# Optimization experiments

Hardware: AMD Instinct MI355X
Metric: run time of the kernel (lower is better)

Reference implementation:

```python
import jax, jax.numpy as jnp
import numpy as np

def setup_inputs() -> dict:
    key = jax.random.key(0)
    k0, k1, k2, k3 = jax.random.split(key, 4)
    B, L, D, E, Dg = 2, 2048, 2048, 8, 256  # Dg = D // E
    x = jax.random.normal(k0, (B, L, D), dtype=jnp.float32)
    Wg = jax.random.normal(k1, (E, D), dtype=jnp.float32) * 0.02     # gate: Linear(D, E)
    Wd = jax.random.normal(k2, (E, Dg, D), dtype=jnp.float32) * 0.02  # down: Linear(D, Dg) per expert
    Wu = jax.random.normal(k3, (E, D, Dg), dtype=jnp.float32) * 0.02  # up:   Linear(Dg, D) per expert
    return {"x": x, "Wg": Wg, "Wd": Wd, "Wu": Wu, "k": 2}

def reference(x, Wg, Wd, Wu, k):
    B, L, D = x.shape
    E = Wg.shape[0]
    T = B * L
    xf = x.reshape(T, D)
    # gate scores: sigmoid(x @ Wg^T), then top-k gate values G and expert indices I
    S = jax.nn.sigmoid(xf @ Wg.T)            # [T, E]
    G, I = jax.lax.top_k(S, k)               # [T, k], [T, k]
    # combine weights per token per expert (zero for unselected experts);
    # equivalent to the original's one_hot + per-expert gather/scatter-add.
    w = jnp.zeros((T, E), x.dtype).at[jnp.arange(T)[:, None], I].add(G)  # [T, E]
    # down: sum_e w[t,e] * (Wd[e] @ x[t])
    down = jnp.einsum('te,egd,td->tg', w, Wd, xf)   # [T, Dg]
    # inner model is identity
    # up: sum_e w[t,e] * (Wu[e] @ down[t])
    up = jnp.einsum('te,edg,tg->td', w, Wu, down)   # [T, D]
    return up.reshape(B, L, D)
```

## Files before the change

### kernel.cpp

```cpp
#include <hip/hip_runtime.h>
#include <stdint.h>

#define T_TOK 4096
#define DIM   2048
#define NEXP  8
#define DG    256
#define TOPK  2

#define BM 64
#define BN 128
#define BKU 64
#define NROWS  (T_TOK*TOPK + NEXP*BM)
#define NBLK_M (NROWS/BM)

typedef __attribute__((ext_vector_type(8))) short short8;
typedef __attribute__((ext_vector_type(4))) float f32x4;

static __device__ __forceinline__ short f2bf(float f) {
    union { float f; uint32_t u; } v{f};
    uint32_t r = v.u + 0x7fffu + ((v.u >> 16) & 1u);
    return (short)(r >> 16);
}
static __device__ __forceinline__ float b2f(short s) {
    union { uint32_t u; float f; } v{((uint32_t)(unsigned short)s) << 16};
    return v.f;
}

#define GLD16(g, l) \
    __builtin_amdgcn_global_load_lds((const __attribute__((address_space(1))) void*)(g), \
                                     (__attribute__((address_space(3))) void*)(l), 16, 0, 0)

__global__ __launch_bounds__(256) void gateconv_kernel(const float* __restrict__ x,
                                                       const float* __restrict__ Wg,
                                                       const float* __restrict__ Wd,
                                                       const float* __restrict__ Wu,
                                                       int* __restrict__ gidx,
                                                       float* __restrict__ gval,
                                                       short* __restrict__ x_bf,
                                                       short* __restrict__ Wd_bf,
                                                       short* __restrict__ Wu_bf)
{
    if (blockIdx.x >= 1024) {
        const int n4 = NEXP * DG * DIM / 4;
        int i = (blockIdx.x - 1024) * 256 + threadIdx.x;
        const float* s; short* d; int j;
        if (i < n4) { s = Wd; d = Wd_bf; j = i; }
        else        { s = Wu; d = Wu_bf; j = i - n4; }
        float4 v = ((const float4*)s)[j];
        short4 o;
        o.x = f2bf(v.x); o.y = f2bf(v.y); o.z = f2bf(v.z); o.w = f2bf(v.w);
        ((short4*)d)[j] = o;
        return;
    }

    int token = blockIdx.x * 4 + (threadIdx.x >> 6);
    int lane  = threadIdx.x & 63;
    const float4* xr = (const float4*)(x + (size_t)token * DIM);

    float4 xv[8];
#pragma unroll
    for (int i = 0; i < 8; i++) xv[i] = xr[lane + 64 * i];

    short4* xb = (short4*)(x_bf + (size_t)token * DIM);
#pragma unroll
    for (int i = 0; i < 8; i++) {
        short4 o;
        o.x = f2bf(xv[i].x); o.y = f2bf(xv[i].y);
        o.z = f2bf(xv[i].z); o.w = f2bf(xv[i].w);
        xb[lane + 64 * i] = o;
    }

    float acc[NEXP];
#pragma unroll
    for (int e = 0; e < NEXP; e++) {
        const float4* wr = (const float4*)(Wg + e * DIM);
        float a = 0.0f;
#pragma unroll
        for (int i = 0; i < 8; i++) {
            float4 w = wr[lane + 64 * i];
            a += xv[i].x * w.x + xv[i].y * w.y + xv[i].z * w.z + xv[i].w * w.w;
        }
        acc[e] = a;
    }

#pragma unroll
    for (int m = 1; m < 64; m <<= 1) {
#pragma unroll
        for (int e = 0; e < NEXP; e++) acc[e] += __shfl_xor(acc[e], m, 64);
    }

    if (lane == 0) {
        float sg[NEXP];
#pragma unroll
        for (int e = 0; e < NEXP; e++) sg[e] = 1.0f / (1.0f + expf(-acc[e]));
        int i0 = 0;
#pragma unroll
        for (int e = 1; e < NEXP; e++) if (sg[e] > sg[i0]) i0 = e;
        int i1 = (i0 == 0) ? 1 : 0;
#pragma unroll
        for (int e = 0; e < NEXP; e++) if (e != i0 && e != i1 && sg[e] > sg[i1]) i1 = e;
        gidx[2 * token + 0] = i0;
        gidx[2 * token + 1] = i1;
        gval[2 * token + 0] = sg[i0];
        gval[2 * token + 1] = sg[i1];
    }
}

__global__ __launch_bounds__(1024) void bucket_kernel(const int* __restrict__ gidx,
                                                      int* __restrict__ rowtok,
                                                      int* __restrict__ rowpos,
                                                      int* __restrict__ seg_off)
{
    __shared__ int cnt[NEXP];
    __shared__ int cur[NEXP];
    int tid = threadIdx.x, lane = tid & 63;
    if (tid < NEXP) cnt[tid] = 0;
    __syncthreads();

    int e_[8];
#pragma unroll
    for (int r = 0; r < 8; r++) e_[r] = gidx[r * 1024 + tid];

    int mycnt = 0;
#pragma unroll
    for (int r = 0; r < 8; r++) {
        int e = e_[r];
#pragma unroll
        for (int ee = 0; ee < NEXP; ee++) {
            unsigned long long m = __ballot(e == ee);
            if (lane == ee) mycnt += (int)__popcll(m);
        }
    }
    if (lane < NEXP) atomicAdd(&cnt[lane], mycnt);
    __syncthreads();

    if (tid == 0) {
        int o = 0;
        for (int e = 0; e < NEXP; e++) {
            seg_off[e] = o;
            cur[e] = o;
            o += ((cnt[e] + BM - 1) / BM) * BM;
        }
        seg_off[NEXP] = o;
    }
    __syncthreads();

    for (int r = tid; r < NROWS; r += 1024) rowtok[r] = -1;
    __syncthreads();

#pragma unroll
    for (int r = 0; r < 8; r++) {
        int idx = r * 1024 + tid;
        int e = e_[r];
#pragma unroll
        for (int ee = 0; ee < NEXP; ee++) {
            unsigned long long m = __ballot(e == ee);
            if (m == 0) continue;
            int leader = __ffsll((unsigned long long)m) - 1;
            int base = 0;
            if (lane == leader) base = atomicAdd(&cur[ee], (int)__popcll(m));
            base = __shfl(base, leader, 64);
            if (e == ee) {
                int pos = base + (int)__popcll(m & ((1ull << lane) - 1ull));
                rowtok[pos] = idx >> 1;
                rowpos[idx] = pos;
            }
        }
    }
}

#define AS3 __attribute__((address_space(3)))

#define VMCNT(N) asm volatile("s_waitcnt vmcnt(" #N ")" ::: "memory")
#define BAR()    __builtin_amdgcn_s_barrier()

#define STAGE(B_) do { \
    GLD16(agA0, lA_##B_##_0); \
    GLD16(agA1, lA_##B_##_1); \
    GLD16(agB0, lB_##B_##_0); \
    GLD16(agB1, lB_##B_##_1); \
    GLD16(agB2, lB_##B_##_2); \
    GLD16(agB3, lB_##B_##_3); \
    agA0 += BKU; agA1 += BKU; \
    agB0 += BKU; agB1 += BKU; agB2 += BKU; agB3 += BKU; \
} while (0)

#define COMP(B_) do { \
    short8 a00 = *(const short8*)&As[B_][am0][c0]; \
    short8 a10 = *(const short8*)&As[B_][am1][c0]; \
    short8 b00 = *(const short8*)&Bs[B_][bn0][c0]; \
    short8 b10 = *(const short8*)&Bs[B_][bn1][c0]; \
    short8 b20 = *(const short8*)&Bs[B_][bn2][c0]; \
    short8 b30 = *(const short8*)&Bs[B_][bn3][c0]; \
    short8 a01 = *(const short8*)&As[B_][am0][c1]; \
    short8 a11 = *(const short8*)&As[B_][am1][c1]; \
    short8 b01 = *(const short8*)&Bs[B_][bn0][c1]; \
    short8 b11 = *(const short8*)&Bs[B_][bn1][c1]; \
    short8 b21 = *(const short8*)&Bs[B_][bn2][c1]; \
    short8 b31 = *(const short8*)&Bs[B_][bn3][c1]; \
    acc[0][0] = __builtin_amdgcn_mfma_f32_16x16x32_bf16(a00, b00, acc[0][0], 0, 0, 0); \
    acc[0][1] = __builtin_amdgcn_mfma_f32_16x16x32_bf16(a00, b10, acc[0][1], 0, 0, 0); \
    acc[0][2] = __builtin_amdgcn_mfma_f32_16x16x32_bf16(a00, b20, acc[0][2], 0, 0, 0); \
    acc[0][3] = __builtin_amdgcn_mfma_f32_16x16x32_bf16(a00, b30, acc[0][3], 0, 0, 0); \
    acc[1][0] = __builtin_amdgcn_mfma_f32_16x16x32_bf16(a10, b00, acc[1][0], 0, 0, 0); \
    acc[1][1] = __builtin_amdgcn_mfma_f32_16x16x32_bf16(a10, b10, acc[1][1], 0, 0, 0); \
    acc[1][2] = __builtin_amdgcn_mfma_f32_16x16x32_bf16(a10, b20, acc[1][2], 0, 0, 0); \
    acc[1][3] = __builtin_amdgcn_mfma_f32_16x16x32_bf16(a10, b30, acc[1][3], 0, 0, 0); \
    acc[0][0] = __builtin_amdgcn_mfma_f32_16x16x32_bf16(a01, b01, acc[0][0], 0, 0, 0); \
    acc[0][1] = __builtin_amdgcn_mfma_f32_16x16x32_bf16(a01, b11, acc[0][1], 0, 0, 0); \
    acc[0][2] = __builtin_amdgcn_mfma_f32_16x16x32_bf16(a01, b21, acc[0][2], 0, 0, 0); \
    acc[0][3] = __builtin_amdgcn_mfma_f32_16x16x32_bf16(a01, b31, acc[0][3], 0, 0, 0); \
    acc[1][0] = __builtin_amdgcn_mfma_f32_16x16x32_bf16(a11, b01, acc[1][0], 0, 0, 0); \
    acc[1][1] = __builtin_amdgcn_mfma_f32_16x16x32_bf16(a11, b11, acc[1][1], 0, 0, 0); \
    acc[1][2] = __builtin_amdgcn_mfma_f32_16x16x32_bf16(a11, b21, acc[1][2], 0, 0, 0); \
    acc[1][3] = __builtin_amdgcn_mfma_f32_16x16x32_bf16(a11, b31, acc[1][3], 0, 0, 0); \
} while (0)

__global__ __launch_bounds__(256) void gemm_down_kernel(const short* __restrict__ A,
                                                        const short* __restrict__ B,
                                                        const int* __restrict__ rowtok,
                                                        const int* __restrict__ seg_off,
                                                        short* __restrict__ C)
{
    constexpr int K = DIM, Ntot = DG;
    __shared__ __align__(16) short As[2][BM][BKU];
    __shared__ __align__(16) short Bs[2][BN][BKU];

    int d = blockIdx.x;
    int lid = (d & 7) * 34 + (d >> 3);
    int bx = lid >> 1, by = lid & 1;

    int row0 = bx * BM;
    int total = seg_off[NEXP];
    if (row0 >= total) return;
    int e = 0;
    while (row0 >= seg_off[e + 1]) ++e;
    int n0 = by * BN;

    int tid = threadIdx.x;
    int w = tid >> 6, l = tid & 63;

    int srow = (w << 3) + (l >> 3);
    int sc   = ((l & 7) ^ ((l >> 3) & 7)) << 3;

    int ta0 = rowtok[row0 + srow];      if (ta0 < 0) ta0 = 0;
    int ta1 = rowtok[row0 + 32 + srow]; if (ta1 < 0) ta1 = 0;
    const short* agA0 = A + (size_t)ta0 * K + sc;
    const short* agA1 = A + (size_t)ta1 * K + sc;
    const short* be = B + (size_t)e * Ntot * K + (size_t)n0 * K;
    const short* agB0 = be + (size_t)(srow     ) * K + sc;
    const short* agB1 = be + (size_t)(srow + 32) * K + sc;
    const short* agB2 = be + (size_t)(srow + 64) * K + sc;
    const short* agB3 = be + (size_t)(srow + 96) * K + sc;

    auto lA_0_0 = (AS3 void*)&As[0][(w << 3)     ][0];
    auto lA_0_1 = (AS3 void*)&As[0][(w << 3) + 32][0];
    auto lA_1_0 = (AS3 void*)&As[1][(w << 3)     ][0];
    auto lA_1_1 = (AS3 void*)&As[1][(w << 3) + 32][0];
    auto lB_0_0 = (AS3 void*)&Bs[0][(w << 3)     ][0];
    auto lB_0_1 = (AS3 void*)&Bs[0][(w << 3) + 32][0];
    auto lB_0_2 = (AS3 void*)&Bs[0][(w << 3) + 64][0];
    auto lB_0_3 = (AS3 void*)&Bs[0][(w << 3) + 96][0];
    auto lB_1_0 = (AS3 void*)&Bs[1][(w << 3)     ][0];
    auto lB_1_1 = (AS3 void*)&Bs[1][(w << 3) + 32][0];
    auto lB_1_2 = (AS3 void*)&Bs[1][(w << 3) + 64][0];
    auto lB_1_3 = (AS3 void*)&Bs[1][(w << 3) + 96][0];

    int mlane = l & 15, qlane = l >> 4;
    int wm = w >> 1, wn = w & 1;
    int c0 = (qlane ^ (mlane & 7)) << 3;
    int c1 = c0 ^ 32;
    int am0 = wm * 32 + mlane, am1 = am0 + 16;
    int bn0 = wn * 64 + mlane, bn1 = bn0 + 16, bn2 = bn0 + 32, bn3 = bn0 + 48;

    f32x4 acc[2][4] = {};

    constexpr int NT = K / BKU;
    STAGE(0);
    STAGE(1);
#pragma unroll 1
    for (int t = 0; t < NT - 2; t += 2) {
        VMCNT(6); BAR();
        COMP(0);
        BAR();
        STAGE(0);
        VMCNT(6); BAR();
        COMP(1);
        BAR();
        if (t + 3 < NT) STAGE(1);
    }
    VMCNT(6); BAR();
    COMP(0);
    BAR();
    VMCNT(0); BAR();
    COMP(1);

#pragma unroll
    for (int i = 0; i < 2; i++) {
        int rbase = row0 + wm * 32 + i * 16 + qlane * 4;
#pragma unroll
        for (int j = 0; j < 4; j++) {
            int col = n0 + wn * 64 + j * 16 + mlane;
#pragma unroll
            for (int r = 0; r < 4; r++)
                C[(size_t)(rbase + r) * Ntot + col] = f2bf(acc[i][j][r]);
        }
    }
}

#undef STAGE

#define STAGE_B(B_) do { \
    GLD16(agB0, lB_##B_##_0); \
    GLD16(agB1, lB_##B_##_1); \
    GLD16(agB2, lB_##B_##_2); \
    GLD16(agB3, lB_##B_##_3); \
    agB0 += BKU; agB1 += BKU; agB2 += BKU; agB3 += BKU; \
} while (0)

#define STAGE_A(B_, kb) do { \
    short8 v0 = *(const short8*)(dr00 + (kb)); \
    short8 v1 = *(const short8*)(dr01 + (kb)); \
    short8 u0 = *(const short8*)(dr10 + (kb)); \
    short8 u1 = *(const short8*)(dr11 + (kb)); \
    short8 o0, o1; \
    _Pragma("unroll") \
    for (int j = 0; j < 8; j++) { \
        o0[j] = f2bf(g00 * b2f(v0[j]) + g01 * b2f(v1[j])); \
        o1[j] = f2bf(g10 * b2f(u0[j]) + g11 * b2f(u1[j])); \
    } \
    *(short8*)&As[B_][srow     ][cl] = o0; \
    *(short8*)&As[B_][srow + 32][cl] = o1; \
} while (0)

__global__ __launch_bounds__(256) void gemm_up_kernel(const short* __restrict__ dr,
                                                      const short* __restrict__ B,
                                                      const int* __restrict__ rowtok,
                                                      const int* __restrict__ rowpos,
                                                      const float* __restrict__ gval,
                                                      const int* __restrict__ seg_off,
                                                      short* __restrict__ C)
{
    constexpr int K = DG, Ntot = DIM;
    __shared__ __align__(16) short As[2][BM][BKU];
    __shared__ __align__(16) short Bs[2][BN][BKU];

    int d = blockIdx.x;
    int lid = (d & 7) * 272 + (d >> 3);
    int bx = lid % NBLK_M;
    int by = lid / NBLK_M;

    int row0 = bx * BM;
    int total = seg_off[NEXP];
    if (row0 >= total) return;
    int e = 0;
    while (row0 >= seg_off[e + 1]) ++e;
    int n0 = by * BN;

    int tid = threadIdx.x;
    int w = tid >> 6, l = tid & 63;

    int srow = (w << 3) + (l >> 3);
    int sc   = ((l & 7) ^ ((l >> 3) & 7)) << 3;
    int cl   = (l & 7) << 3;

    int t0 = rowtok[row0 + srow];      if (t0 < 0) t0 = 0;
    int t1 = rowtok[row0 + 32 + srow]; if (t1 < 0) t1 = 0;
    int   p00 = rowpos[2 * t0], p01 = rowpos[2 * t0 + 1];
    int   p10 = rowpos[2 * t1], p11 = rowpos[2 * t1 + 1];
    float g00 = gval[2 * t0],   g01 = gval[2 * t0 + 1];
    float g10 = gval[2 * t1],   g11 = gval[2 * t1 + 1];
    const short* dr00 = dr + (size_t)p00 * DG + sc;
    const short* dr01 = dr + (size_t)p01 * DG + sc;
    const short* dr10 = dr + (size_t)p10 * DG + sc;
    const short* dr11 = dr + (size_t)p11 * DG + sc;

    const short* be = B + (size_t)e * Ntot * K + (size_t)n0 * K;
    const short* agB0 = be + (size_t)(srow     ) * K + sc;
    const short* agB1 = be + (size_t)(srow + 32) * K + sc;
    const short* agB2 = be + (size_t)(srow + 64) * K + sc;
    const short* agB3 = be + (size_t)(srow + 96) * K + sc;

    auto lB_0_0 = (AS3 void*)&Bs[0][(w << 3)     ][0];
    auto lB_0_1 = (AS3 void*)&Bs[0][(w << 3) + 32][0];
    auto lB_0_2 = (AS3 void*)&Bs[0][(w << 3) + 64][0];
    auto lB_0_3 = (AS3 void*)&Bs[0][(w << 3) + 96][0];
    auto lB_1_0 = (AS3 void*)&Bs[1][(w << 3)     ][0];
    auto lB_1_1 = (AS3 void*)&Bs[1][(w << 3) + 32][0];
    auto lB_1_2 = (AS3 void*)&Bs[1][(w << 3) + 64][0];
    auto lB_1_3 = (AS3 void*)&Bs[1][(w << 3) + 96][0];

    int mlane = l & 15, qlane = l >> 4;
    int wm = w >> 1, wn = w & 1;
    int c0 = (qlane ^ (mlane & 7)) << 3;
    int c1 = c0 ^ 32;
    int am0 = wm * 32 + mlane, am1 = am0 + 16;
    int bn0 = wn * 64 + mlane, bn1 = bn0 + 16, bn2 = bn0 + 32, bn3 = bn0 + 48;

    f32x4 acc[2][4] = {};

    STAGE_A(0, 0); STAGE_B(0);
    __syncthreads();
    STAGE_A(1, BKU); STAGE_B(1);
    COMP(0);
    __syncthreads();
    STAGE_A(0, 2 * BKU); STAGE_B(0);
    COMP(1);
    __syncthreads();
    STAGE_A(1, 3 * BKU); STAGE_B(1);
    COMP(0);
    __syncthreads();
    COMP(1);

#pragma unroll
    for (int i = 0; i < 2; i++) {
        int rbase = row0 + wm * 32 + i * 16 + qlane * 4;
#pragma unroll
        for (int j = 0; j < 4; j++) {
            int col = n0 + wn * 64 + j * 16 + mlane;
#pragma unroll
            for (int r = 0; r < 4; r++)
                C[(size_t)(rbase + r) * Ntot + col] = f2bf(acc[i][j][r]);
        }
    }
}

#undef STAGE_A
#undef STAGE_B
#undef COMP
#undef AS3

__global__ __launch_bounds__(256) void combine2_kernel(const short* __restrict__ ur,
                                                       const int* __restrict__ rowpos,
                                                       const float* __restrict__ gval,
                                                       float* __restrict__ out)
{
    int i = blockIdx.x * 256 + threadIdx.x;
    int t = i >> 9;
    int c = (i & 511) * 4;
    int   p0 = rowpos[2 * t], p1 = rowpos[2 * t + 1];
    float g0 = gval[2 * t],   g1 = gval[2 * t + 1];
    short4 u0 = *(const short4*)&ur[(size_t)p0 * DIM + c];
    short4 u1 = *(const short4*)&ur[(size_t)p1 * DIM + c];
    float4 o;
    o.x = g0 * b2f(u0.x) + g1 * b2f(u1.x);
    o.y = g0 * b2f(u0.y) + g1 * b2f(u1.y);
    o.z = g0 * b2f(u0.z) + g1 * b2f(u1.z);
    o.w = g0 * b2f(u0.w) + g1 * b2f(u1.w);
    *(float4*)&out[(size_t)t * DIM + c] = o;
}

extern "C" void kernel_launch(void* const* d_in, const int* in_sizes, int n_in,
                              void* d_out, int out_size, void* d_ws, size_t ws_size,
                              hipStream_t stream) {
    const float* x  = (const float*)d_in[0];
    const float* Wg = (const float*)d_in[1];
    const float* Wd = (const float*)d_in[2];
    const float* Wu = (const float*)d_in[3];
    float* out = (float*)d_out;

    char* p = (char*)d_ws;
    int*   gidx    = (int*)(p + 0);
    float* gval    = (float*)(p + 32768);
    int*   rowtok  = (int*)(p + 65536);
    int*   rowpos  = (int*)(p + 100352);
    int*   seg_off = (int*)(p + 133120);
    short* x_bf    = (short*)(p + 133376);
    short* Wd_bf   = (short*)(p + 133376 + 16777216);
    short* Wu_bf   = Wd_bf + 4194304;
    short* dr_bf   = Wu_bf + 4194304;
    short* ur_bf   = dr_bf + (size_t)NROWS * DG;

    gateconv_kernel<<<9216, 256, 0, stream>>>(x, Wg, Wd, Wu, gidx, gval, x_bf, Wd_bf, Wu_bf);
    bucket_kernel<<<1, 1024, 0, stream>>>(gidx, rowtok, rowpos, seg_off);
    gemm_down_kernel<<<NBLK_M * (DG / BN), 256, 0, stream>>>(x_bf, Wd_bf, rowtok, seg_off, dr_bf);
    gemm_up_kernel<<<NBLK_M * (DIM / BN), 256, 0, stream>>>(dr_bf, Wu_bf, rowtok, rowpos, gval, seg_off, ur_bf);
    combine2_kernel<<<T_TOK * DIM / 4 / 256, 256, 0, stream>>>(ur_bf, rowpos, gval, out);
}
```

Baseline: 204.0 us.

## Split-K down GEMM with fp32 atomics and fuse combine into up-GEMM epilogue

Splits the down-projection GEMM four ways along K, accumulating partial results with fp32 atomics into a zeroed buffer, so more blocks can run in parallel. The up-projection epilogue now scales each row by its gate value and atomically adds straight into the output, which removes the bf16 intermediate and the separate combine kernel. Zeroing of the output and down buffers is folded into the existing conversion kernel. The cost is atomic traffic on a 4096x2048 fp32 output and fp32 rather than bf16 loads of the down activations.

```diff
diff --git a/kernel.cpp b/kernel.cpp
--- a/kernel.cpp
+++ b/kernel.cpp
@@ -12,8 +12,10 @@
 #define BKU 64
 #define NROWS  (T_TOK*TOPK + NEXP*BM)
 #define NBLK_M (NROWS/BM)
+#define KSPLIT 4
 
 typedef __attribute__((ext_vector_type(8))) short short8;
+typedef __attribute__((ext_vector_type(8))) float float8;
 typedef __attribute__((ext_vector_type(4))) float f32x4;
 
 static __device__ __forceinline__ short f2bf(float f) {
@@ -38,8 +40,21 @@
                                                        float* __restrict__ gval,
                                                        short* __restrict__ x_bf,
                                                        short* __restrict__ Wd_bf,
-                                                       short* __restrict__ Wu_bf)
+                                                       short* __restrict__ Wu_bf,
+                                                       float* __restrict__ out,
+                                                       float* __restrict__ dr)
 {
+    if (blockIdx.x >= 9216) {
+        int z = blockIdx.x - 9216;
+        float4 zero = {0.f, 0.f, 0.f, 0.f};
+#pragma unroll
+        for (int q = 0; q < 4; q++) {
+            int i = z * 1024 + q * 256 + threadIdx.x;
+            if (i < 2097152) ((float4*)out)[i] = zero;
+            else             ((float4*)dr)[i - 2097152] = zero;
+        }
+        return;
+    }
     if (blockIdx.x >= 1024) {
         const int n4 = NEXP * DG * DIM / 4;
         int i = (blockIdx.x - 1024) * 256 + threadIdx.x;
@@ -107,8 +122,10 @@
 }
 
 __global__ __launch_bounds__(1024) void bucket_kernel(const int* __restrict__ gidx,
+                                                      const float* __restrict__ gval,
                                                       int* __restrict__ rowtok,
                                                       int* __restrict__ rowpos,
+                                                      float* __restrict__ grow,
                                                       int* __restrict__ seg_off)
 {
     __shared__ int cnt[NEXP];
@@ -164,6 +181,7 @@
                 int pos = base + (int)__popcll(m & ((1ull << lane) - 1ull));
                 rowtok[pos] = idx >> 1;
                 rowpos[idx] = pos;
+                grow[pos] = gval[idx];
             }
         }
     }
@@ -220,14 +238,17 @@
                                                         const short* __restrict__ B,
                                                         const int* __restrict__ rowtok,
                                                         const int* __restrict__ seg_off,
-                                                        short* __restrict__ C)
+                                                        float* __restrict__ dr)
 {
     constexpr int K = DIM, Ntot = DG;
+    constexpr int KCHUNK = K / KSPLIT;
     __shared__ __align__(16) short As[2][BM][BKU];
     __shared__ __align__(16) short Bs[2][BN][BKU];
 
-    int d = blockIdx.x;
-    int lid = (d & 7) * 34 + (d >> 3);
+    int d  = blockIdx.x;
+    int ks = d / 272;
+    int q  = d % 272;
+    int lid = (q & 7) * 34 + (q >> 3);
     int bx = lid >> 1, by = lid & 1;
 
     int row0 = bx * BM;
@@ -236,6 +257,7 @@
     int e = 0;
     while (row0 >= seg_off[e + 1]) ++e;
     int n0 = by * BN;
+    int kb = ks * KCHUNK;
 
     int tid = threadIdx.x;
     int w = tid >> 6, l = tid & 63;
@@ -245,9 +267,9 @@
 
     int ta0 = rowtok[row0 + srow];      if (ta0 < 0) ta0 = 0;
     int ta1 = rowtok[row0 + 32 + srow]; if (ta1 < 0) ta1 = 0;
-    const short* agA0 = A + (size_t)ta0 * K + sc;
-    const short* agA1 = A + (size_t)ta1 * K + sc;
-    const short* be = B + (size_t)e * Ntot * K + (size_t)n0 * K;
+    const short* agA0 = A + (size_t)ta0 * K + kb + sc;
+    const short* agA1 = A + (size_t)ta1 * K + kb + sc;
+    const short* be = B + (size_t)e * Ntot * K + (size_t)n0 * K + kb;
     const short* agB0 = be + (size_t)(srow     ) * K + sc;
     const short* agB1 = be + (size_t)(srow + 32) * K + sc;
     const short* agB2 = be + (size_t)(srow + 64) * K + sc;
@@ -275,7 +297,7 @@
 
     f32x4 acc[2][4] = {};
 
-    constexpr int NT = K / BKU;
+    constexpr int NT = KCHUNK / BKU;
     STAGE(0);
     STAGE(1);
 #pragma unroll 1
@@ -303,7 +325,7 @@
             int col = n0 + wn * 64 + j * 16 + mlane;
 #pragma unroll
             for (int r = 0; r < 4; r++)
-                C[(size_t)(rbase + r) * Ntot + col] = f2bf(acc[i][j][r]);
+                atomicAdd(&dr[(size_t)(rbase + r) * Ntot + col], acc[i][j][r]);
         }
     }
 }
@@ -319,27 +341,28 @@
 } while (0)
 
 #define STAGE_A(B_, kb) do { \
-    short8 v0 = *(const short8*)(dr00 + (kb)); \
-    short8 v1 = *(const short8*)(dr01 + (kb)); \
-    short8 u0 = *(const short8*)(dr10 + (kb)); \
-    short8 u1 = *(const short8*)(dr11 + (kb)); \
+    float8 v0 = *(const float8*)(dr00 + (kb)); \
+    float8 v1 = *(const float8*)(dr01 + (kb)); \
+    float8 u0 = *(const float8*)(dr10 + (kb)); \
+    float8 u1 = *(const float8*)(dr11 + (kb)); \
     short8 o0, o1; \
     _Pragma("unroll") \
     for (int j = 0; j < 8; j++) { \
-        o0[j] = f2bf(g00 * b2f(v0[j]) + g01 * b2f(v1[j])); \
-        o1[j] = f2bf(g10 * b2f(u0[j]) + g11 * b2f(u1[j])); \
+        o0[j] = f2bf(g00 * v0[j] + g01 * v1[j]); \
+        o1[j] = f2bf(g10 * u0[j] + g11 * u1[j]); \
     } \
     *(short8*)&As[B_][srow     ][cl] = o0; \
     *(short8*)&As[B_][srow + 32][cl] = o1; \
 } while (0)
 
-__global__ __launch_bounds__(256) void gemm_up_kernel(const short* __restrict__ dr,
+__global__ __launch_bounds__(256) void gemm_up_kernel(const float* __restrict__ dr,
                                                       const short* __restrict__ B,
                                                       const int* __restrict__ rowtok,
                                                       const int* __restrict__ rowpos,
                                                       const float* __restrict__ gval,
+                                                      const float* __restrict__ grow,
                                                       const int* __restrict__ seg_off,
-                                                      short* __restrict__ C)
+                                                      float* __restrict__ out)
 {
     constexpr int K = DG, Ntot = DIM;
     __shared__ __align__(16) short As[2][BM][BKU];
@@ -370,10 +393,10 @@
     int   p10 = rowpos[2 * t1], p11 = rowpos[2 * t1 + 1];
     float g00 = gval[2 * t0],   g01 = gval[2 * t0 + 1];
     float g10 = gval[2 * t1],   g11 = gval[2 * t1 + 1];
-    const short* dr00 = dr + (size_t)p00 * DG + sc;
-    const short* dr01 = dr + (size_t)p01 * DG + sc;
-    const short* dr10 = dr + (size_t)p10 * DG + sc;
-    const short* dr11 = dr + (size_t)p11 * DG + sc;
+    const float* dr00 = dr + (size_t)p00 * DG + sc;
+    const float* dr01 = dr + (size_t)p01 * DG + sc;
+    const float* dr10 = dr + (size_t)p10 * DG + sc;
+    const float* dr11 = dr + (size_t)p11 * DG + sc;
 
     const short* be = B + (size_t)e * Ntot * K + (size_t)n0 * K;
     const short* agB0 = be + (size_t)(srow     ) * K + sc;
@@ -416,11 +439,15 @@
     for (int i = 0; i < 2; i++) {
         int rbase = row0 + wm * 32 + i * 16 + qlane * 4;
 #pragma unroll
-        for (int j = 0; j < 4; j++) {
-            int col = n0 + wn * 64 + j * 16 + mlane;
-#pragma unroll
-            for (int r = 0; r < 4; r++)
-                C[(size_t)(rbase + r) * Ntot + col] = f2bf(acc[i][j][r]);
+        for (int r = 0; r < 4; r++) {
+            int row = rbase + r;
+            int tt = rowtok[row];
+            if (tt < 0) continue;
+            float g = grow[row];
+            float* orow = out + (size_t)tt * Ntot + n0 + wn * 64 + mlane;
+#pragma unroll
+            for (int j = 0; j < 4; j++)
+                atomicAdd(orow + j * 16, g * acc[i][j][r]);
         }
     }
 }
@@ -429,26 +456,6 @@
 #undef STAGE_B
 #undef COMP
 #undef AS3
-
-__global__ __launch_bounds__(256) void combine2_kernel(const short* __restrict__ ur,
-                                                       const int* __restrict__ rowpos,
-                                                       const float* __restrict__ gval,
-                                                       float* __restrict__ out)
-{
-    int i = blockIdx.x * 256 + threadIdx.x;
-    int t = i >> 9;
-    int c = (i & 511) * 4;
-    int   p0 = rowpos[2 * t], p1 = rowpos[2 * t + 1];
-    float g0 = gval[2 * t],   g1 = gval[2 * t + 1];
-    short4 u0 = *(const short4*)&ur[(size_t)p0 * DIM + c];
-    short4 u1 = *(const short4*)&ur[(size_t)p1 * DIM + c];
-    float4 o;
-    o.x = g0 * b2f(u0.x) + g1 * b2f(u1.x);
-    o.y = g0 * b2f(u0.y) + g1 * b2f(u1.y);
-    o.z = g0 * b2f(u0.z) + g1 * b2f(u1.z);
-    o.w = g0 * b2f(u0.w) + g1 * b2f(u1.w);
-    *(float4*)&out[(size_t)t * DIM + c] = o;
-}
 
 extern "C" void kernel_launch(void* const* d_in, const int* in_sizes, int n_in,
                               void* d_out, int out_size, void* d_ws, size_t ws_size,
@@ -465,15 +472,14 @@
     int*   rowtok  = (int*)(p + 65536);
     int*   rowpos  = (int*)(p + 100352);
     int*   seg_off = (int*)(p + 133120);
-    short* x_bf    = (short*)(p + 133376);
-    short* Wd_bf   = (short*)(p + 133376 + 16777216);
+    float* grow    = (float*)(p + 133376);
+    short* x_bf    = (short*)(p + 168192);
+    short* Wd_bf   = (short*)(p + 168192 + 16777216);
     short* Wu_bf   = Wd_bf + 4194304;
-    short* dr_bf   = Wu_bf + 4194304;
-    short* ur_bf   = dr_bf + (size_t)NROWS * DG;
-
-    gateconv_kernel<<<9216, 256, 0, stream>>>(x, Wg, Wd, Wu, gidx, gval, x_bf, Wd_bf, Wu_bf);
-    bucket_kernel<<<1, 1024, 0, stream>>>(gidx, rowtok, rowpos, seg_off);
-    gemm_down_kernel<<<NBLK_M * (DG / BN), 256, 0, stream>>>(x_bf, Wd_bf, rowtok, seg_off, dr_bf);
-    gemm_up_kernel<<<NBLK_M * (DIM / BN), 256, 0, stream>>>(dr_bf, Wu_bf, rowtok, rowpos, gval, seg_off, ur_bf);
-    combine2_kernel<<<T_TOK * DIM / 4 / 256, 256, 0, stream>>>(ur_bf, rowpos, gval, out);
-}
+    float* dr      = (float*)(p + 168192 + 16777216 + 2 * 8388608);
+
+    gateconv_kernel<<<11808, 256, 0, stream>>>(x, Wg, Wd, Wu, gidx, gval, x_bf, Wd_bf, Wu_bf, out, dr);
+    bucket_kernel<<<1, 1024, 0, stream>>>(gidx, gval, rowtok, rowpos, grow, seg_off);
+    gemm_down_kernel<<<NBLK_M * 2 * KSPLIT, 256, 0, stream>>>(x_bf, Wd_bf, rowtok, seg_off, dr);
+    gemm_up_kernel<<<NBLK_M * (DIM / BN), 256, 0, stream>>>(dr, Wu_bf, rowtok, rowpos, gval, grow, seg_off, out);
+}
```

After: 264.0 us. 1.29x slower.
